# Kernel tuning notes

Measured on AMD Instinct MI355X. Metric: run time of the kernel, lower is better.

The kernel has to match this reference:

```python
import jax, jax.numpy as jnp
from jax import lax
import numpy as np

P = 7            # patch_size
NP = 10          # n_patches
WIN = 20         # window_size
STRIDE = 4       # window loop stride
EMB = 128        # embedding_dimension
L = WIN - P + 1  # valid-conv output side (14)
HALF = WIN // 2 - P // 2  # window start offset before clipping (7)


def _positions(H, W):
    # x outer, y inner, exactly matching the nested python loops in the source
    return np.array([(x, y) for x in range(0, H - WIN + 1, STRIDE)
                     for y in range(0, W - WIN + 1, STRIDE)], dtype=np.int32)


def _forward(images, Wp, bp, pos_emb, Wb, bb):
    B, C, H, W = images.shape
    BC = B * C
    pos = jnp.asarray(_positions(H, W))  # [Ppos, 2]

    def per_pos(p):
        x, y = p[0], p[1]
        xb0 = jnp.maximum(x - HALF, 0)          # clipped window start (x / cols)
        yb0 = jnp.maximum(y - HALF, 0)          # clipped window start (y / rows)
        winW = jnp.minimum(x - HALF + WIN, W) - xb0  # clipped window width
        winH = jnp.minimum(y - HALF + WIN, H) - yb0  # clipped window height
        # reference patch: rows y:y+P, cols x:x+P (from ORIGINAL data, as in source)
        ref = lax.dynamic_slice(images, (0, 0, y, x), (B, C, P, P)).reshape(BC, 1, P, P)
        # fixed-size window slice; upper bound never clips for our dims, lower-clip
        # handled by masking invalid candidate offsets below
        win = lax.dynamic_slice(images, (0, 0, yb0, xb0), (B, C, WIN, WIN)).reshape(BC, WIN, WIN)
        # grouped cross-correlation == torch conv2d(groups=BC) similarity
        sim = lax.conv_general_dilated(win[None], ref, (1, 1), 'VALID',
                                       feature_group_count=BC,
                                       dimension_numbers=('NCHW', 'OIHW', 'NCHW'))[0]  # [BC,L,L]
        valid = (jnp.arange(L)[:, None] <= winH - P) & (jnp.arange(L)[None, :] <= winW - P)
        sim = jnp.where(valid[None], sim, -jnp.inf)
        _, idx = lax.top_k(sim.reshape(BC, L * L), NP)  # [BC, NP]
        oy, ox = idx // L, idx % L  # row / col offsets inside the window

        def extract(w2, a, b):
            # source's meshgrid indexing yields the TRANSPOSED patch, flattened
            return lax.dynamic_slice(w2, (a, b), (P, P)).T.reshape(P * P)
        patches = jax.vmap(jax.vmap(extract, in_axes=(None, 0, 0)))(win, oy, ox)  # [BC,NP,P*P]
        # source bug kept: x_coords = row offset + x window start (and vice versa)
        return patches, oy + xb0, ox + yb0

    patches, xi, yi = jax.vmap(per_pos)(pos)  # [Ppos,BC,NP,49], [Ppos,BC,NP] int32 x2

    # NOTE: the TransformerEncoder output is discarded in the source; the actual
    # math is back_projection(projection(patches) + pos_emb).
    emb = patches.reshape(-1, B, C, NP, P * P) @ Wp + bp + pos_emb  # [Ppos,B,C,NP,EMB]
    den = (emb @ Wb + bb).reshape(-1, BC, NP, P, P)                 # [Ppos,BC,NP,P,P]

    img0 = images.reshape(BC, H, W)
    cnt0 = jnp.ones((BC, H, W), images.dtype)

    def upd(im, cn, x_i, y_i, d):
        reg = lax.dynamic_slice(im, (y_i, x_i), (P, P))
        c = lax.dynamic_slice(cn, (y_i, x_i), (P, P))
        im = lax.dynamic_update_slice(im, (reg * c + d) / (c + 1.0), (y_i, x_i))
        # source bug kept: counter incremented at transposed slice [x, y]
        ct = lax.dynamic_slice(cn, (x_i, y_i), (P, P)) + 1.0
        cn = lax.dynamic_update_slice(cn, ct, (x_i, y_i))
        return im, cn
    vupd = jax.vmap(upd)  # (b,c) planes are independent -> vectorize

    def n_step(carry, t):
        d, x_i, y_i = t
        return vupd(carry[0], carry[1], x_i, y_i, d), None

    def pos_step(carry, t):
        d, x_i, y_i = t  # d:[BC,NP,P,P]
        carry, _ = lax.scan(n_step, carry, (jnp.moveaxis(d, 1, 0), x_i.T, y_i.T))
        return carry, None

    (img, _), _ = lax.scan(pos_step, (img0, cnt0), (den, xi, yi))
    return img.reshape(B, C, H, W)


def setup_inputs() -> dict:
    key = jax.random.key(0)
    k0, k1, k2, k3 = jax.random.split(key, 4)
    B, C, H, W = 4, 8, 160, 160
    return {
        'images': jax.random.normal(k0, (B, C, H, W), jnp.float32),
        'Wp': jax.random.normal(k1, (P * P, EMB), jnp.float32) * 0.05,
        'bp': jnp.zeros((EMB,), jnp.float32),
        'pos_emb': jax.random.normal(k2, (1, NP, EMB), jnp.float32),
        'Wb': jax.random.normal(k3, (EMB, P * P), jnp.float32) * 0.05,
        'bb': jnp.zeros((P * P,), jnp.float32),
    }


def reference(images, Wp, bp, pos_emb, Wb, bb):
    return _forward(images, Wp, bp, pos_emb, Wb, bb)
```

## Files before the change

### kernel.cpp

```cpp
#include <hip/hip_runtime.h>

#define PS 7
#define NP 10
#define WIN 20
#define STR 4
#define LL 14
#define HALF 7
#define HH 160
#define WW 160
#define BCN 32
#define NX 36
#define PPOS 1296
#define EMBD 128
#define NTASK (BCN * PPOS * NP)
#define NEV (PPOS * NP)
#define CAP 512
#define NTILE 400

__global__ __launch_bounds__(256) void k_mk(const float* __restrict__ Wp,
                                            const float* __restrict__ bp,
                                            const float* __restrict__ pe,
                                            const float* __restrict__ Wb,
                                            const float* __restrict__ bb,
                                            float* __restrict__ M2,
                                            float* __restrict__ K,
                                            unsigned long long* __restrict__ MT) {
    int t = blockIdx.x * 256 + threadIdx.x;
    if (t < 49 * 49) {
        int d = t / 49, j = t % 49;
        float acc = 0.f;
        for (int e = 0; e < EMBD; ++e) acc += Wp[j * EMBD + e] * Wb[e * 49 + d];
        M2[t] = acc;
    } else if (t < 49 * 49 + NP * 49) {
        int u = t - 49 * 49;
        int n = u / 49, d = u % 49;
        float acc = bb[d];
        for (int e = 0; e < EMBD; ++e) acc += (bp[e] + pe[n * EMBD + e]) * Wb[e * 49 + d];
        K[u] = acc;
    } else if (t < 49 * 49 + NP * 49 + 256) {
        int u = t - (49 * 49 + NP * 49);
        int ey = (u >> 4) - 7, ex = (u & 15) - 7;
        int r0 = ey > 0 ? ey : 0, r1 = ey + 6 < 7 ? ey + 6 : 7;
        int c0 = ex > 0 ? ex : 0, c1 = ex + 6 < 7 ? ex + 6 : 7;
        unsigned long long m = 0ull;
        if (r0 <= r1 && c0 <= c1) {
            unsigned colp = ((1u << (c1 - c0 + 1)) - 1u) << c0;
            for (int rr = r0; rr <= r1; ++rr)
                m |= (unsigned long long)colp << (8 * rr);
        }
        MT[u] = m;
    }
}

__device__ __forceinline__ float dpp_wave_max(float x) {
    int xi = __float_as_int(x);
#define DPP_STEP(ctrl)                                                          \
    {                                                                           \
        int t_ = __builtin_amdgcn_update_dpp(xi, xi, ctrl, 0xf, 0xf, false);    \
        xi = __float_as_int(fmaxf(__int_as_float(xi), __int_as_float(t_)));     \
    }
    DPP_STEP(0x111)
    DPP_STEP(0x112)
    DPP_STEP(0x114)
    DPP_STEP(0x118)
    DPP_STEP(0x142)
    DPP_STEP(0x143)
#undef DPP_STEP
    return __int_as_float(xi);
}

__device__ __forceinline__ int dpp_scan_add(int x) {
    int t;
    t = __builtin_amdgcn_update_dpp(0, x, 0x111, 0xf, 0xf, true);  x += t;
    t = __builtin_amdgcn_update_dpp(0, x, 0x112, 0xf, 0xf, true);  x += t;
    t = __builtin_amdgcn_update_dpp(0, x, 0x114, 0xf, 0xf, true);  x += t;
    t = __builtin_amdgcn_update_dpp(0, x, 0x118, 0xf, 0xf, true);  x += t;
    t = __builtin_amdgcn_update_dpp(0, x, 0x142, 0xa, 0xf, false); x += t;
    t = __builtin_amdgcn_update_dpp(0, x, 0x143, 0xc, 0xf, false); x += t;
    return x;
}

__global__ __launch_bounds__(256) void k_sim(const float* __restrict__ img,
                                             unsigned* __restrict__ xy) {
    int tid  = threadIdx.x;
    int wv   = __builtin_amdgcn_readfirstlane(tid >> 6);
    int lane = tid & 63;
    int gt   = blockIdx.x * 4 + wv;
    int pos  = gt % PPOS;
    int bc   = gt / PPOS;
    int ix = pos / NX, iy = pos % NX;
    int x = ix * STR, y = iy * STR;
    int xb0 = max(x - HALF, 0), yb0 = max(y - HALF, 0);
    int jmax = x + 6 - xb0;
    int imax = y + 6 - yb0;
    const float* plane = img + bc * (HH * WW);

    float rf[49];
#pragma unroll
    for (int a = 0; a < PS; ++a)
#pragma unroll
        for (int b = 0; b < PS; ++b)
            rf[a * 7 + b] = plane[(y + a) * WW + (x + b)];

    int B = lane;
    bool bval = B < 56;
    int gr = B / 14, c = B % 14;
    int r0 = gr * 4;
    float acc[4] = {0.f, 0.f, 0.f, 0.f};
    const float* wb = plane + yb0 * WW + xb0 + c;
#pragma unroll
    for (int a = 0; a < 10; ++a) {
        int ra = min(r0 + a, 19);
        const float* rp = wb + ra * WW;
#pragma unroll
        for (int b = 0; b < 7; ++b) {
            float tap = rp[b];
#pragma unroll
            for (int k = 0; k < 4; ++k) {
                int ai = a - k;
                if (ai >= 0 && ai < 7) acc[k] += tap * rf[ai * 7 + b];
            }
        }
    }
    float v[4]; int vidx[4];
#pragma unroll
    for (int k = 0; k < 4; ++k) {
        int rr = r0 + k;
        bool ok = bval && (rr <= imax) && (c <= jmax);
        v[k] = ok ? acc[k] : -INFINITY;
        vidx[k] = rr * 14 + c;
    }

    int tbase = (bc * PPOS + pos) * NP;

    for (int n = 0; n < NP; ++n) {
        float bv = fmaxf(fmaxf(v[0], v[1]), fmaxf(v[2], v[3]));
        bv = dpp_wave_max(bv);
        float bvs = __int_as_float(__builtin_amdgcn_readlane(__float_as_int(bv), 63));
        unsigned long long ms[4];
        ms[0] = __ballot(v[0] == bvs);
        ms[1] = __ballot(v[1] == bvs);
        ms[2] = __ballot(v[2] == bvs);
        ms[3] = __ballot(v[3] == bvs);
        int best = 1 << 30, slotw = 0, lanew = 0;
#pragma unroll
        for (int s = 0; s < 4; ++s) {
            if (ms[s]) {
                int l  = __ffsll(ms[s]) - 1;
                int id = __builtin_amdgcn_readlane(vidx[s], l);
                if (id < best) { best = id; slotw = s; lanew = l; }
            }
        }
#pragma unroll
        for (int s = 0; s < 4; ++s)
            if (s == slotw && lane == lanew) v[s] = -INFINITY;

        int oy = best / 14, ox = best % 14;
        int x_i = oy + xb0;
        int y_i = ox + yb0;
        if (lane == 0) xy[tbase + n] = (unsigned)x_i | ((unsigned)y_i << 8);
    }
}

__global__ __launch_bounds__(256) void k_den(const float* __restrict__ img,
                                             const unsigned* __restrict__ xy,
                                             const float* __restrict__ M2,
                                             const float* __restrict__ Kg,
                                             float* __restrict__ pd) {
    __shared__ float xb[4][64 * 49];
    int tid  = threadIdx.x;
    int wv   = tid >> 6;
    int lane = tid & 63;
    int t = blockIdx.x * 256 + tid;
    int n = t % NP;
    int q = t / NP;
    int pos = q % PPOS;
    int bc  = q / PPOS;
    int ix = pos / NX, iy = pos % NX;
    int x = ix * STR, y = iy * STR;
    int xb0 = max(x - HALF, 0), yb0 = max(y - HALF, 0);
    unsigned u = xy[t];
    int x_i = (int)(u & 255u), y_i = (int)((u >> 8) & 255u);
    const float* src = img + bc * (HH * WW) + (yb0 + x_i - xb0) * WW + (xb0 + y_i - yb0);

    float tap[49];
#pragma unroll
    for (int j = 0; j < 49; ++j) tap[j] = src[(j % 7) * WW + (j / 7)];

    const float* kp = Kg + n * 49;
    float* xbuf = xb[wv];
    for (int d = 0; d < 49; ++d) {
        const float* mrow = M2 + d * 49;
        float a0 = 0.f, a1 = 0.f;
#pragma unroll
        for (int j = 0; j < 48; j += 2) {
            a0 = fmaf(tap[j],     mrow[j],     a0);
            a1 = fmaf(tap[j + 1], mrow[j + 1], a1);
        }
        a0 = fmaf(tap[48], mrow[48], a0);
        xbuf[lane * 49 + d] = (a0 + a1) + kp[d];
    }
    size_t base = (size_t)(blockIdx.x * 256 + wv * 64) * 49;
#pragma unroll
    for (int i = 0; i < 49; ++i)
        pd[base + i * 64 + lane] = xbuf[i * 64 + lane];
}

__global__ __launch_bounds__(128) void k_apply(const float* __restrict__ img,
                                               const unsigned* __restrict__ xy,
                                               const float* __restrict__ pd,
                                               const unsigned long long* __restrict__ mt,
                                               float* __restrict__ out) {
    __shared__ __align__(16) uint2 lsts[2][CAP];
    int tid  = threadIdx.x;
    int wv   = tid >> 6;
    int lane = tid & 63;
    int bs   = (blockIdx.x & 7) * 800 + (blockIdx.x >> 3);
    int gt   = bs * 2 + wv;
    int bc   = gt / NTILE;
    int tile = gt % NTILE;
    int tx0 = (tile % 20) * 8, ty0 = (tile / 20) * 8;
    int tx1 = tx0 + 7, ty1 = ty0 + 7;
    const unsigned* xs = xy + bc * NEV;
    uint2* lst = lsts[wv];

    int a0 = (tx0 <= 19) ? 0 : ((tx0 - 9) >> 2), a1 = min(35, (tx0 + 14) >> 2);
    int b0 = (ty0 <= 19) ? 0 : ((ty0 - 9) >> 2), b1 = min(35, (ty0 + 14) >> 2);
    if (a0 > b0) { int t0 = a0; a0 = b0; b0 = t0; int t1 = a1; a1 = b1; b1 = t1; }
    int lo0 = a0, lo1 = 0, len0, len1;
    if (b0 <= a1 + 1) { len0 = max(a1, b1) - lo0 + 1; len1 = 0; }
    else              { len0 = a1 - a0 + 1; lo1 = b0; len1 = b1 - b0 + 1; }
    int nU = len0 + len1;
    unsigned m = 65536u / (unsigned)nU + 1u;
    int npos = nU * nU;

    unsigned cnt = 0;
    for (int base = 0; base < npos; base += 64) {
        int k = base + lane;
        bool valid = k < npos;
        unsigned kk = valid ? (unsigned)k : 0u;
        int ki = (int)((kk * m) >> 16);
        int kj = (int)kk - ki * nU;
        int ixp = (ki < len0) ? (lo0 + ki) : (lo1 + ki - len0);
        int iyp = (kj < len0) ? (lo0 + kj) : (lo1 + kj - len0);
        int pos = ixp * NX + iyp;
        const unsigned* ep = xs + pos * NP;

        unsigned ev[NP];
#pragma unroll
        for (int n = 0; n < NP; ++n) ev[n] = ep[n];

        unsigned rel = 0;
        unsigned w0[NP], w1[NP];
#pragma unroll
        for (int n = 0; n < NP; ++n) {
            unsigned u = ev[n];
            int x_i = (int)(u & 255u);
            int y_i = (int)((u >> 8) & 255u);
            int exH = x_i - tx0, eyH = y_i - ty0;
            int eyC = x_i - ty0, exC = y_i - tx0;
            bool ih = ((unsigned)(exH + 6) <= 13u) & ((unsigned)(eyH + 6) <= 13u);
            bool ch = ((unsigned)(eyC + 6) <= 13u) & ((unsigned)(exC + 6) <= 13u);
            bool any = valid && (ih || ch);
            rel |= any ? (1u << n) : 0u;
            unsigned hidx = ih ? (unsigned)(((eyH + 7) << 4) | (exH + 7)) : 0u;
            unsigned cidx = ch ? (unsigned)(((eyC + 7) << 4) | (exC + 7)) : 0u;
            unsigned s8q  = ih ? (unsigned)(((7 * eyH + exH) + 48) << 2) : 0u;
            w0[n] = (unsigned)(pos * NP + n);
            w1[n] = hidx | (cidx << 8) | (s8q << 16);
        }
        int myc  = __popc(rel);
        int scan = dpp_scan_add(myc);
        int total = __builtin_amdgcn_readlane(scan, 63);
        int excl  = (int)cnt + scan - myc;
        int w = excl;
#pragma unroll
        for (int n = 0; n < NP; ++n) {
            if ((rel >> n) & 1u) { if (w < CAP) lst[w] = make_uint2(w0[n], w1[n]); ++w; }
        }
        cnt += (unsigned)total;
    }
    if (cnt > CAP) cnt = CAP;
    unsigned cntp = (cnt + 7u) & ~7u;
    if (cntp > CAP) cntp = CAP;
    if (lane < (int)(cntp - cnt)) lst[cnt + lane] = make_uint2(0u, 0u);
    int cntN = (int)cntp;

    int r8 = lane >> 3, c8 = lane & 7;
    int r  = ty0 + r8;
    int cc = tx0 + c8;
    float im = img[bc * (HH * WW) + r * WW + cc];
    float c  = 1.0f;
    const float* ds = pd + (size_t)bc * ((size_t)NEV * 49);
    int vOff2 = (r8 * 7 + c8) * 4 + 192;

    for (int i = 0; i < cntN; i += 8) {
        unsigned u0[8], u1[8];
        float    dv[8];
#pragma unroll
        for (int j = 0; j < 4; ++j) {
            uint4 e2 = *reinterpret_cast<const uint4*>(&lst[i + 2 * j]);
            u0[2 * j]     = (unsigned)__builtin_amdgcn_readfirstlane((int)e2.x);
            u1[2 * j]     = (unsigned)__builtin_amdgcn_readfirstlane((int)e2.y);
            u0[2 * j + 1] = (unsigned)__builtin_amdgcn_readfirstlane((int)e2.z);
            u1[2 * j + 1] = (unsigned)__builtin_amdgcn_readfirstlane((int)e2.w);
        }
        unsigned long long hm[8], cm[8];
#pragma unroll
        for (int j = 0; j < 8; ++j) {
            hm[j] = mt[u1[j] & 255u];
            cm[j] = mt[(u1[j] >> 8) & 255u];
        }
#pragma unroll
        for (int j = 0; j < 8; ++j) {
            int t_ = (int)(u0[j] & 16383u);
            const char* dsb = (const char*)(ds + (size_t)t_ * 49);
            int boc = vOff2 - (int)((u1[j] >> 16) & 511u);
            dv[j] = *(const float*)(dsb + boc);
        }
        float inc[8], cv[8], rv[8];
#pragma unroll
        for (int j = 0; j < 8; ++j)
            asm("v_cndmask_b32 %0, 0, 1.0, %1" : "=v"(inc[j]) : "s"(cm[j]));
        cv[0] = c;
#pragma unroll
        for (int j = 1; j < 8; ++j) cv[j] = cv[j - 1] + inc[j - 1];
        c = cv[7] + inc[7];
#pragma unroll
        for (int j = 0; j < 8; ++j) rv[j] = __builtin_amdgcn_rcpf(cv[j] + 1.0f);
#pragma unroll
        for (int j = 0; j < 8; ++j) {
            float nim = fmaf(im, cv[j], dv[j]) * rv[j];
            asm("v_cndmask_b32 %0, %0, %1, %2" : "+v"(im) : "v"(nim), "s"(hm[j]));
        }
    }
    out[bc * (HH * WW) + r * WW + cc] = im;
}

extern "C" void kernel_launch(void* const* d_in, const int* in_sizes, int n_in,
                              void* d_out, int out_size, void* d_ws, size_t ws_size,
                              hipStream_t stream) {
    const float* img = (const float*)d_in[0];
    const float* Wp  = (const float*)d_in[1];
    const float* bp  = (const float*)d_in[2];
    const float* pe  = (const float*)d_in[3];
    const float* Wb  = (const float*)d_in[4];
    const float* bb  = (const float*)d_in[5];
    float* out = (float*)d_out;

    float* wsf = (float*)d_ws;
    float*              M2 = wsf;
    float*              K  = wsf + 2404;
    unsigned long long* MT = (unsigned long long*)(wsf + 2896);
    unsigned*           xy = (unsigned*)(wsf + 3408);
    float*              pd = wsf + 3408 + NTASK;

    k_mk<<<13, 256, 0, stream>>>(Wp, bp, pe, Wb, bb, M2, K, MT);
    k_sim<<<BCN * PPOS / 4, 256, 0, stream>>>(img, xy);
    k_den<<<NTASK / 256, 256, 0, stream>>>(img, xy, M2, K, pd);
    k_apply<<<BCN * NTILE / 2, 128, 0, stream>>>(img, xy, pd, MT, out);
}
```

Measured before the change: 289.4 us.

## Fuse patch denoise projection into similarity/top-k kernel using LDS window

Removes the separate k_den kernel and computes each selected patch's 49-dim denoised output inside k_sim right after top-k selection. Each wave stages its 20x20 window in shared memory and keeps one column of the 49x49 projection matrix per lane in registers. The M matrix layout is transposed so each lane computes one output dimension. This avoids an extra kernel launch, a global reload of xy and the patch taps, and the k_den shared-memory staging, at the cost of more registers in k_sim, which may lower occupancy, and serialized per-n dot products per wave.

```diff
diff --git a/kernel.cpp b/kernel.cpp
--- a/kernel.cpp
+++ b/kernel.cpp
@@ -22,15 +22,15 @@
                                             const float* __restrict__ pe,
                                             const float* __restrict__ Wb,
                                             const float* __restrict__ bb,
-                                            float* __restrict__ M2,
+                                            float* __restrict__ M,
                                             float* __restrict__ K,
                                             unsigned long long* __restrict__ MT) {
     int t = blockIdx.x * 256 + threadIdx.x;
     if (t < 49 * 49) {
-        int d = t / 49, j = t % 49;
+        int k = t / 49, d = t % 49;
         float acc = 0.f;
-        for (int e = 0; e < EMBD; ++e) acc += Wp[j * EMBD + e] * Wb[e * 49 + d];
-        M2[t] = acc;
+        for (int e = 0; e < EMBD; ++e) acc += Wp[k * EMBD + e] * Wb[e * 49 + d];
+        M[t] = acc;
     } else if (t < 49 * 49 + NP * 49) {
         int u = t - 49 * 49;
         int n = u / 49, d = u % 49;
@@ -81,7 +81,11 @@
 }
 
 __global__ __launch_bounds__(256) void k_sim(const float* __restrict__ img,
-                                             unsigned* __restrict__ xy) {
+                                             const float* __restrict__ Mg,
+                                             const float* __restrict__ Kg,
+                                             unsigned* __restrict__ xy,
+                                             float* __restrict__ pd) {
+    __shared__ float winb[4][400];
     int tid  = threadIdx.x;
     int wv   = __builtin_amdgcn_readfirstlane(tid >> 6);
     int lane = tid & 63;
@@ -94,6 +98,14 @@
     int jmax = x + 6 - xb0;
     int imax = y + 6 - yb0;
     const float* plane = img + bc * (HH * WW);
+    float* winw = winb[wv];
+
+#pragma unroll
+    for (int i0 = 0; i0 < 448; i0 += 64) {
+        int i = i0 + lane;
+        if (i < 400) winw[i] = plane[(yb0 + i / 20) * WW + (xb0 + i % 20)];
+    }
+    __syncthreads();
 
     float rf[49];
 #pragma unroll
@@ -131,6 +143,12 @@
         vidx[k] = rr * 14 + c;
     }
 
+    int ld = min(lane, 48);
+    float Mc[49];
+#pragma unroll
+    for (int j = 0; j < 49; ++j) Mc[j] = Mg[j * 49 + ld];
+
+    bool act = lane < 49;
     int tbase = (bc * PPOS + pos) * NP;
 
     for (int n = 0; n < NP; ++n) {
@@ -158,52 +176,27 @@
         int oy = best / 14, ox = best % 14;
         int x_i = oy + xb0;
         int y_i = ox + yb0;
-        if (lane == 0) xy[tbase + n] = (unsigned)x_i | ((unsigned)y_i << 8);
-    }
-}
-
-__global__ __launch_bounds__(256) void k_den(const float* __restrict__ img,
-                                             const unsigned* __restrict__ xy,
-                                             const float* __restrict__ M2,
-                                             const float* __restrict__ Kg,
-                                             float* __restrict__ pd) {
-    __shared__ float xb[4][64 * 49];
-    int tid  = threadIdx.x;
-    int wv   = tid >> 6;
-    int lane = tid & 63;
-    int t = blockIdx.x * 256 + tid;
-    int n = t % NP;
-    int q = t / NP;
-    int pos = q % PPOS;
-    int bc  = q / PPOS;
-    int ix = pos / NX, iy = pos % NX;
-    int x = ix * STR, y = iy * STR;
-    int xb0 = max(x - HALF, 0), yb0 = max(y - HALF, 0);
-    unsigned u = xy[t];
-    int x_i = (int)(u & 255u), y_i = (int)((u >> 8) & 255u);
-    const float* src = img + bc * (HH * WW) + (yb0 + x_i - xb0) * WW + (xb0 + y_i - yb0);
-
-    float tap[49];
-#pragma unroll
-    for (int j = 0; j < 49; ++j) tap[j] = src[(j % 7) * WW + (j / 7)];
-
-    const float* kp = Kg + n * 49;
-    float* xbuf = xb[wv];
-    for (int d = 0; d < 49; ++d) {
-        const float* mrow = M2 + d * 49;
-        float a0 = 0.f, a1 = 0.f;
-#pragma unroll
-        for (int j = 0; j < 48; j += 2) {
-            a0 = fmaf(tap[j],     mrow[j],     a0);
-            a1 = fmaf(tap[j + 1], mrow[j + 1], a1);
-        }
-        a0 = fmaf(tap[48], mrow[48], a0);
-        xbuf[lane * 49 + d] = (a0 + a1) + kp[d];
-    }
-    size_t base = (size_t)(blockIdx.x * 256 + wv * 64) * 49;
-#pragma unroll
-    for (int i = 0; i < 49; ++i)
-        pd[base + i * 64 + lane] = xbuf[i * 64 + lane];
+        int t = tbase + n;
+        if (lane == 0) xy[t] = (unsigned)x_i | ((unsigned)y_i << 8);
+
+        const float* tb = winw + oy * 20 + ox;
+        float tap[49];
+#pragma unroll
+        for (int j = 0; j < 49; ++j)
+            tap[j] = tb[(j % 7) * 20 + (j / 7)];
+
+        float d0 = Kg[n * 49 + ld], d1 = 0.f, d2 = 0.f, d3 = 0.f;
+#pragma unroll
+        for (int j = 0; j < 48; j += 4) {
+            d0 = fmaf(tap[j + 0], Mc[j + 0], d0);
+            d1 = fmaf(tap[j + 1], Mc[j + 1], d1);
+            d2 = fmaf(tap[j + 2], Mc[j + 2], d2);
+            d3 = fmaf(tap[j + 3], Mc[j + 3], d3);
+        }
+        d0 = fmaf(tap[48], Mc[48], d0);
+        float den = (d0 + d1) + (d2 + d3);
+        if (act) pd[(size_t)t * 49 + lane] = den;
+    }
 }
 
 __global__ __launch_bounds__(128) void k_apply(const float* __restrict__ img,
@@ -349,14 +342,13 @@
     float* out = (float*)d_out;
 
     float* wsf = (float*)d_ws;
-    float*              M2 = wsf;
+    float*              M  = wsf;
     float*              K  = wsf + 2404;
     unsigned long long* MT = (unsigned long long*)(wsf + 2896);
     unsigned*           xy = (unsigned*)(wsf + 3408);
     float*              pd = wsf + 3408 + NTASK;
 
-    k_mk<<<13, 256, 0, stream>>>(Wp, bp, pe, Wb, bb, M2, K, MT);
-    k_sim<<<BCN * PPOS / 4, 256, 0, stream>>>(img, xy);
-    k_den<<<NTASK / 256, 256, 0, stream>>>(img, xy, M2, K, pd);
+    k_mk<<<13, 256, 0, stream>>>(Wp, bp, pe, Wb, bb, M, K, MT);
+    k_sim<<<BCN * PPOS / 4, 256, 0, stream>>>(img, M, K, xy, pd);
     k_apply<<<BCN * NTILE / 2, 128, 0, stream>>>(img, xy, pd, MT, out);
 }
```

Result: no change. 287.4 us (-0.7%).
